# Performance work log

Hardware: AMD Instinct MI355X
Metric: run time of the kernel (lower is better)

## Reference

```python
import jax, jax.numpy as jnp
import numpy as np

B, S, E, H = 4, 2048, 1024, 16
D = E // H
MAX_DIST = 4
LN_EPS = 1e-5


def setup_inputs() -> dict:
    key = jax.random.key(0)
    ks = jax.random.split(key, 12)
    std = 1.0 / np.sqrt(E)
    inp = {
        "x": jax.random.normal(ks[0], (B, S, E), dtype=jnp.float32),
        "distances": jax.random.randint(ks[1], (B, S, S), 0, 5, dtype=jnp.int64),
        "Wq": jax.random.normal(ks[2], (E, E), dtype=jnp.float32) * std,
        "bq": jnp.zeros((E,), dtype=jnp.float32),
        "Wk": jax.random.normal(ks[3], (E, E), dtype=jnp.float32) * std,
        "bk": jnp.zeros((E,), dtype=jnp.float32),
        "Wv": jax.random.normal(ks[4], (E, E), dtype=jnp.float32) * std,
        "bv": jnp.zeros((E,), dtype=jnp.float32),
        "Wo": jax.random.normal(ks[5], (E, E), dtype=jnp.float32) * std,
        "bo": jnp.zeros((E,), dtype=jnp.float32),
        "dist_bias": jax.random.normal(ks[6], (MAX_DIST + 1,), dtype=jnp.float32) * 0.1,
        "ln_g": jnp.ones((E,), dtype=jnp.float32),
        "ln_b": jnp.zeros((E,), dtype=jnp.float32),
    }
    return inp


def _layernorm(y, g, b):
    mu = jnp.mean(y, axis=-1, keepdims=True)
    var = jnp.mean(jnp.square(y - mu), axis=-1, keepdims=True)
    return (y - mu) * jax.lax.rsqrt(var + LN_EPS) * g + b


def reference(x, distances, Wq, bq, Wk, bk, Wv, bv, Wo, bo, dist_bias, ln_g, ln_b):
    scale = 1.0 / np.sqrt(D)
    # projections (torch Linear: x @ W.T + b), split into heads -> [B,H,S,D]
    def heads(y):
        return y.reshape(B, S, H, D).transpose(0, 2, 1, 3)
    q = heads(x @ Wq.T + bq)
    k = heads(x @ Wk.T + bk)
    v = heads(x @ Wv.T + bv)
    scores = jnp.einsum('bhsd,bhtd->bhst', q, k) * scale  # [B,H,S,S]
    d = jnp.clip(distances, 0, MAX_DIST)
    bias = dist_bias[d]  # [B,S,S] gather from learned table
    scores = scores + bias[:, None, :, :]
    attn = jax.nn.softmax(scores, axis=-1)
    out = jnp.einsum('bhst,bhtd->bhsd', attn, v)
    out = out.transpose(0, 2, 1, 3).reshape(B, S, E)
    out = out @ Wo.T + bo
    return _layernorm(x + out, ln_g, ln_b)
```

## Files before the change

kernel.cpp:

```cpp
#include <hip/hip_runtime.h>
#include <stdint.h>

#define NB 4
#define NS 2048
#define NE 1024
#define NH 16
#define ND 64
#define LN_EPS 1e-5f
#define LN2I 1.44269504089f

typedef __attribute__((ext_vector_type(8))) unsigned short u16x8;
typedef __attribute__((ext_vector_type(4))) unsigned short u16x4;
typedef __attribute__((ext_vector_type(8))) short b16x8;
typedef __attribute__((ext_vector_type(4))) float f32x4;

static __device__ __forceinline__ unsigned short f2bf(float f) {
  unsigned u = __builtin_bit_cast(unsigned, f);
  u += 0x7FFFu + ((u >> 16) & 1u);
  return (unsigned short)(u >> 16);
}
static __device__ __forceinline__ float bf2f(unsigned short h) {
  return __builtin_bit_cast(float, (unsigned)h << 16);
}
static __device__ __forceinline__ float bperm_f(int addr, float v) {
  return __builtin_bit_cast(float,
      __builtin_amdgcn_ds_bpermute(addr, __builtin_bit_cast(int, v)));
}
static __device__ __forceinline__ unsigned cvtpk(float lo, float hi) {
  unsigned r;
  asm("v_cvt_pk_bf16_f32 %0, %1, %2" : "=v"(r) : "v"(lo), "v"(hi));
  return r;
}
#if __has_builtin(__builtin_amdgcn_exp2f)
static __device__ __forceinline__ float ex2(float x) { return __builtin_amdgcn_exp2f(x); }
#else
static __device__ __forceinline__ float ex2(float x) { return exp2f(x); }
#endif

static __device__ __forceinline__ void gload16(const unsigned short* gsrc,
                                               unsigned short* ldsbase) {
  __builtin_amdgcn_global_load_lds(
      (__attribute__((address_space(1))) unsigned int*)(uintptr_t)gsrc,
      (__attribute__((address_space(3))) unsigned int*)(uintptr_t)ldsbase,
      16, 0, 0);
}

#define MFMA16(a, b, c) __builtin_amdgcn_mfma_f32_16x16x32_bf16( \
    __builtin_bit_cast(b16x8, a), __builtin_bit_cast(b16x8, b), c, 0, 0, 0)

__global__ void k_cvt(const float* __restrict__ src, unsigned short* __restrict__ dst, int n) {
  int i = (blockIdx.x * 256 + threadIdx.x) * 8;
  if (i >= n) return;
  float4 a = *(const float4*)(src + i);
  float4 b = *(const float4*)(src + i + 4);
  u16x8 o;
  o[0]=f2bf(a.x); o[1]=f2bf(a.y); o[2]=f2bf(a.z); o[3]=f2bf(a.w);
  o[4]=f2bf(b.x); o[5]=f2bf(b.y); o[6]=f2bf(b.z); o[7]=f2bf(b.w);
  *(u16x8*)(dst + i) = o;
}

__global__ void k_bias(const int* __restrict__ d, const float* __restrict__ tbl,
                       unsigned short* __restrict__ bias) {
  size_t i = ((size_t)blockIdx.x * 256 + threadIdx.x) * 8;
  int4 a = *(const int4*)(d + i);
  int4 b = *(const int4*)(d + i + 4);
  u16x8 o;
  int v;
  v = a.x; v = v < 0 ? 0 : (v > 4 ? 4 : v); o[0] = f2bf(tbl[v] * LN2I);
  v = a.y; v = v < 0 ? 0 : (v > 4 ? 4 : v); o[1] = f2bf(tbl[v] * LN2I);
  v = a.z; v = v < 0 ? 0 : (v > 4 ? 4 : v); o[2] = f2bf(tbl[v] * LN2I);
  v = a.w; v = v < 0 ? 0 : (v > 4 ? 4 : v); o[3] = f2bf(tbl[v] * LN2I);
  v = b.x; v = v < 0 ? 0 : (v > 4 ? 4 : v); o[4] = f2bf(tbl[v] * LN2I);
  v = b.y; v = v < 0 ? 0 : (v > 4 ? 4 : v); o[5] = f2bf(tbl[v] * LN2I);
  v = b.z; v = v < 0 ? 0 : (v > 4 ? 4 : v); o[6] = f2bf(tbl[v] * LN2I);
  v = b.w; v = v < 0 ? 0 : (v > 4 ? 4 : v); o[7] = f2bf(tbl[v] * LN2I);
  *(u16x8*)(bias + i) = o;
}

__global__ __launch_bounds__(256, 3) void k_qkv(
    const unsigned short* __restrict__ xb,
    const unsigned short* __restrict__ wq, const unsigned short* __restrict__ wk_,
    const unsigned short* __restrict__ wv,
    const float* __restrict__ bq, const float* __restrict__ bk_, const float* __restrict__ bv,
    unsigned short* __restrict__ q, unsigned short* __restrict__ kk,
    unsigned short* __restrict__ vt) {
  __shared__ unsigned short sA[128 * 64];
  __shared__ unsigned short sB[128 * 64];
  const int tid = threadIdx.x;
  const int lane = tid & 63, wid = tid >> 6;
  const int g = lane >> 4, c16 = lane & 15;
  const int wm = wid >> 1, wn = wid & 1;
  const int z = blockIdx.z;
  const unsigned short* w = (z == 0) ? wq : ((z == 1) ? wk_ : wv);
  const float* bias = (z == 0) ? bq : ((z == 1) ? bk_ : bv);
  const int n0 = blockIdx.x * 128, m0 = blockIdx.y * 128;

  f32x4 acc[4][4];
#pragma unroll
  for (int i = 0; i < 4; ++i)
#pragma unroll
    for (int j = 0; j < 4; ++j) acc[i][j] = f32x4{0.f, 0.f, 0.f, 0.f};

  const int crow = lane >> 3, gcol8 = (lane & 7) * 8;

  for (int k0 = 0; k0 < NE; k0 += 64) {
#pragma unroll
    for (int i = 0; i < 4; ++i) {
      int c = wid * 4 + i;
      int row = c * 8 + crow;
      gload16(xb + (size_t)(m0 + row) * NE + k0 + gcol8, &sA[c * 512]);
      gload16(w + (size_t)(n0 + row) * NE + k0 + gcol8, &sB[c * 512]);
    }
    __syncthreads();
#pragma unroll
    for (int dc = 0; dc < 2; ++dc) {
      u16x8 af[4], bf[4];
#pragma unroll
      for (int mt = 0; mt < 4; ++mt)
        af[mt] = *(const u16x8*)(sA + (wm * 64 + mt * 16 + c16) * 64 + dc * 32 + g * 8);
#pragma unroll
      for (int nt = 0; nt < 4; ++nt)
        bf[nt] = *(const u16x8*)(sB + (wn * 64 + nt * 16 + c16) * 64 + dc * 32 + g * 8);
#pragma unroll
      for (int mt = 0; mt < 4; ++mt)
#pragma unroll
        for (int nt = 0; nt < 4; ++nt)
          acc[mt][nt] = MFMA16(af[mt], bf[nt], acc[mt][nt]);
    }
    __syncthreads();
  }

  if (z == 0) {
#pragma unroll
    for (int mt = 0; mt < 4; ++mt)
#pragma unroll
      for (int nt = 0; nt < 4; ++nt) {
        int col = n0 + wn * 64 + nt * 16 + c16;
        float bb = bias[col];
#pragma unroll
        for (int rr = 0; rr < 4; ++rr) {
          int row = m0 + wm * 64 + mt * 16 + g * 4 + rr;
          q[(size_t)row * NE + col] = f2bf(acc[mt][nt][rr] + bb);
        }
      }
  } else if (z == 1) {
#pragma unroll
    for (int mt = 0; mt < 4; ++mt)
#pragma unroll
      for (int nt = 0; nt < 4; ++nt) {
        int col = n0 + wn * 64 + nt * 16 + c16;
        float bb = bias[col];
        int seg = col & ~63, d = col & 63;
#pragma unroll
        for (int rr = 0; rr < 4; ++rr) {
          int row = m0 + wm * 64 + mt * 16 + g * 4 + rr;
          int dsw = (((d >> 3) ^ (row & 7)) << 3) | (d & 7);
          kk[(size_t)row * NE + seg + dsw] = f2bf(acc[mt][nt][rr] + bb);
        }
      }
  } else {
#pragma unroll
    for (int mt = 0; mt < 4; ++mt)
#pragma unroll
      for (int nt = 0; nt < 4; ++nt) {
        int col = n0 + wn * 64 + nt * 16 + c16;
        float bb = bias[col];
        int h = col >> 6, dd = col & 63;
        int grow = m0 + wm * 64 + mt * 16 + g * 4;
        int b = grow >> 11, ss = grow & 2047;
        int ssw = (ss & ~63) | (((((ss >> 3) & 7) ^ (dd & 7)) << 3)) | (ss & 7);
        u16x4 o;
#pragma unroll
        for (int rr = 0; rr < 4; ++rr) o[rr] = f2bf(acc[mt][nt][rr] + bb);
        *(u16x4*)(vt + ((size_t)((b * NH + h) * ND + dd)) * NS + ssw) = o;
      }
  }
}

__global__ __launch_bounds__(256, 2) void k_attn(
    const unsigned short* __restrict__ q, const unsigned short* __restrict__ kk,
    const unsigned short* __restrict__ vt, const unsigned short* __restrict__ bias,
    unsigned short* __restrict__ attn) {
  __shared__ unsigned short sK[2][64 * 64];
  __shared__ unsigned short sV[2][64 * 64];
  __shared__ unsigned short sP[4][16 * 64];
  const int tid = threadIdx.x, lane = tid & 63, wid = tid >> 6;
  const int g = lane >> 4, c16 = lane & 15;
  const int flat = blockIdx.x;
  const int kdec = flat >> 3;
  const int h = kdec & 15;
  const int G = (flat & 7) | ((kdec >> 4) << 3);
  const int b = G >> 3, qb = G & 7;
  const int q0 = qb * 256 + wid * 64;
  const size_t qkbase = ((size_t)b * NS) * NE + (size_t)h * ND;
  const size_t vbase = ((size_t)(b * NH + h) * ND) * NS;
  const size_t bbase = (size_t)b * NS * NS;
  unsigned short* sPw = &sP[wid][0];

  u16x8 qf[4][2];
#pragma unroll
  for (int mt = 0; mt < 4; ++mt)
#pragma unroll
    for (int dc = 0; dc < 2; ++dc)
      qf[mt][dc] = *(const u16x8*)(q + qkbase + (size_t)(q0 + mt * 16 + c16) * NE + dc * 32 + g * 8);

  f32x4 oa[4][4];
  float l[4];
#pragma unroll
  for (int mt = 0; mt < 4; ++mt) {
#pragma unroll
    for (int dt = 0; dt < 4; ++dt) oa[mt][dt] = f32x4{0.f, 0.f, 0.f, 0.f};
    l[mt] = 0.f;
  }

  int addr_rr[4];
#pragma unroll
  for (int rr = 0; rr < 4; ++rr) addr_rr[rr] = (g * 20 + rr) * 4;

  const int crow = lane >> 3, gcol8 = (lane & 7) * 8;
  const int rs0 = (g ^ (c16 & 7)) << 3;
  const int rs1 = ((4 + g) ^ (c16 & 7)) << 3;
  const int pw_base = c16 * 64 + (g & 1) * 4;
  const int pr0 = c16 * 64 + ((g ^ (c16 & 7)) << 3);
  const int pr1 = c16 * 64 + (((4 + g) ^ (c16 & 7)) << 3);

  u16x4 bp[4][4];

  auto stage = [&](int kt, int ib) {
#pragma unroll
    for (int i = 0; i < 4; ++i) {
      int c = wid * 4 + i;
      if (c < 8)
        gload16(kk + qkbase + (size_t)(kt + c * 8 + crow) * NE + gcol8, &sK[ib][c * 512]);
      else
        gload16(vt + vbase + (size_t)((c - 8) * 8 + crow) * NS + kt + gcol8, &sV[ib][(c - 8) * 512]);
    }
  };

  stage(0, 0);
#pragma unroll
  for (int mt = 0; mt < 4; ++mt)
#pragma unroll
    for (int nt = 0; nt < 4; ++nt)
      bp[mt][nt] = *(const u16x4*)(bias + bbase +
          (size_t)(q0 + mt * 16 + c16) * NS + 0 + nt * 16 + g * 4);

  for (int kt = 0, it = 0; kt < NS; kt += 64, ++it) {
    __syncthreads();
    if (kt + 64 < NS) stage(kt + 64, (it + 1) & 1);
    const unsigned short* bK = &sK[it & 1][0];
    const unsigned short* bV = &sV[it & 1][0];

    u16x8 kf[4][2];
#pragma unroll
    for (int nt = 0; nt < 4; ++nt) {
      const unsigned short* kr = bK + (nt * 16 + c16) * 64;
      kf[nt][0] = *(const u16x8*)(kr + rs0);
      kf[nt][1] = *(const u16x8*)(kr + rs1);
    }

#pragma unroll
    for (int mt = 0; mt < 4; ++mt) {
      f32x4 p[4];
      __builtin_amdgcn_s_setprio(1);
#pragma unroll
      for (int nt = 0; nt < 4; ++nt) {
        f32x4 t = f32x4{0.f, 0.f, 0.f, 0.f};
        t = MFMA16(kf[nt][0], qf[mt][0], t);
        t = MFMA16(kf[nt][1], qf[mt][1], t);
        p[nt] = t;
      }
      __builtin_amdgcn_s_setprio(0);
      float rs = 0.f;
#pragma unroll
      for (int nt = 0; nt < 4; ++nt)
#pragma unroll
        for (int rr = 0; rr < 4; ++rr) {
          float e = ex2(p[nt][rr] * (0.125f * LN2I) + bf2f(bp[mt][nt][rr]));
          p[nt][rr] = e;
          rs += e;
        }
      rs += __shfl_xor(rs, 16);
      rs += __shfl_xor(rs, 32);
      l[mt] += rs;
#pragma unroll
      for (int nt = 0; nt < 4; ++nt) {
        unsigned w0 = cvtpk(p[nt][0], p[nt][1]);
        unsigned w1 = cvtpk(p[nt][2], p[nt][3]);
        *(unsigned long long*)(sPw + pw_base + (((2 * nt + (g >> 1)) ^ (c16 & 7)) << 3)) =
            ((unsigned long long)w1 << 32) | (unsigned long long)w0;
      }
      if (mt == 1 && kt + 64 < NS) {
#pragma unroll
        for (int m2 = 0; m2 < 2; ++m2)
#pragma unroll
          for (int nt = 0; nt < 4; ++nt)
            bp[m2][nt] = *(const u16x4*)(bias + bbase +
                (size_t)(q0 + m2 * 16 + c16) * NS + kt + 64 + nt * 16 + g * 4);
      }
      if (mt == 3 && kt + 64 < NS) {
#pragma unroll
        for (int m2 = 0; m2 < 2; ++m2)
#pragma unroll
          for (int nt = 0; nt < 4; ++nt)
            bp[2 + m2][nt] = *(const u16x4*)(bias + bbase +
                (size_t)(q0 + (2 + m2) * 16 + c16) * NS + kt + 64 + nt * 16 + g * 4);
      }
      __builtin_amdgcn_s_setprio(1);
#pragma unroll
      for (int h2 = 0; h2 < 2; ++h2) {
        u16x8 pa = *(const u16x8*)(sPw + (h2 ? pr1 : pr0));
#pragma unroll
        for (int dt = 0; dt < 4; ++dt) {
          u16x8 vb = *(const u16x8*)(bV + (dt * 16 + c16) * 64 + (h2 ? rs1 : rs0));
          oa[mt][dt] = MFMA16(pa, vb, oa[mt][dt]);
        }
      }
      __builtin_amdgcn_s_setprio(0);
    }
  }

#pragma unroll
  for (int mt = 0; mt < 4; ++mt) {
    float invl = 1.0f / l[mt];
    float invr[4];
#pragma unroll
    for (int rr = 0; rr < 4; ++rr) invr[rr] = bperm_f(addr_rr[rr], invl);
#pragma unroll
    for (int dt = 0; dt < 4; ++dt)
#pragma unroll
      for (int rr = 0; rr < 4; ++rr) {
        int row = q0 + mt * 16 + g * 4 + rr;
        attn[qkbase + (size_t)row * NE + dt * 16 + c16] = f2bf(oa[mt][dt][rr] * invr[rr]);
      }
  }
}

__global__ __launch_bounds__(256, 3) void k_proj(
    const unsigned short* __restrict__ a, const unsigned short* __restrict__ w,
    const float* __restrict__ bo, const float* __restrict__ x, float* __restrict__ y) {
  __shared__ unsigned short sA[128 * 64];
  __shared__ unsigned short sB[128 * 64];
  const int tid = threadIdx.x;
  const int lane = tid & 63, wid = tid >> 6;
  const int g = lane >> 4, c16 = lane & 15;
  const int wm = wid >> 1, wn = wid & 1;
  const int n0 = blockIdx.x * 128, m0 = blockIdx.y * 128;

  f32x4 acc[4][4];
#pragma unroll
  for (int i = 0; i < 4; ++i)
#pragma unroll
    for (int j = 0; j < 4; ++j) acc[i][j] = f32x4{0.f, 0.f, 0.f, 0.f};

  const int crow = lane >> 3, gcol8 = (lane & 7) * 8;

  for (int k0 = 0; k0 < NE; k0 += 64) {
#pragma unroll
    for (int i = 0; i < 4; ++i) {
      int c = wid * 4 + i;
      int row = c * 8 + crow;
      gload16(a + (size_t)(m0 + row) * NE + k0 + gcol8, &sA[c * 512]);
      gload16(w + (size_t)(n0 + row) * NE + k0 + gcol8, &sB[c * 512]);
    }
    __syncthreads();
#pragma unroll
    for (int dc = 0; dc < 2; ++dc) {
      u16x8 af[4], bf[4];
#pragma unroll
      for (int mt = 0; mt < 4; ++mt)
        af[mt] = *(const u16x8*)(sA + (wm * 64 + mt * 16 + c16) * 64 + dc * 32 + g * 8);
#pragma unroll
      for (int nt = 0; nt < 4; ++nt)
        bf[nt] = *(const u16x8*)(sB + (wn * 64 + nt * 16 + c16) * 64 + dc * 32 + g * 8);
#pragma unroll
      for (int mt = 0; mt < 4; ++mt)
#pragma unroll
        for (int nt = 0; nt < 4; ++nt)
          acc[mt][nt] = MFMA16(af[mt], bf[nt], acc[mt][nt]);
    }
    __syncthreads();
  }

#pragma unroll
  for (int mt = 0; mt < 4; ++mt)
#pragma unroll
    for (int nt = 0; nt < 4; ++nt) {
      int col = n0 + wn * 64 + nt * 16 + c16;
      float bb = bo[col];
#pragma unroll
      for (int rr = 0; rr < 4; ++rr) {
        int row = m0 + wm * 64 + mt * 16 + g * 4 + rr;
        y[(size_t)row * NE + col] = acc[mt][nt][rr] + bb + x[(size_t)row * NE + col];
      }
    }
}

__global__ void k_ln(const float* __restrict__ y, const float* __restrict__ gg,
                     const float* __restrict__ bb, float* __restrict__ out) {
  const int row = blockIdx.x, tid = threadIdx.x;
  float4 v = *(const float4*)(y + (size_t)row * NE + tid * 4);
  float s = v.x + v.y + v.z + v.w;
  float s2 = v.x * v.x + v.y * v.y + v.z * v.z + v.w * v.w;
#pragma unroll
  for (int off = 1; off < 64; off <<= 1) {
    s += __shfl_xor(s, off);
    s2 += __shfl_xor(s2, off);
  }
  __shared__ float red[8];
  const int wid = tid >> 6, lane = tid & 63;
  if (lane == 0) { red[wid * 2] = s; red[wid * 2 + 1] = s2; }
  __syncthreads();
  s = red[0] + red[2] + red[4] + red[6];
  s2 = red[1] + red[3] + red[5] + red[7];
  float mu = s * (1.0f / NE);
  float var = s2 * (1.0f / NE) - mu * mu;
  float rstd = rsqrtf(var + LN_EPS);
  float4 g4 = *(const float4*)(gg + tid * 4);
  float4 b4 = *(const float4*)(bb + tid * 4);
  float4 o;
  o.x = (v.x - mu) * rstd * g4.x + b4.x;
  o.y = (v.y - mu) * rstd * g4.y + b4.y;
  o.z = (v.z - mu) * rstd * g4.z + b4.z;
  o.w = (v.w - mu) * rstd * g4.w + b4.w;
  *(float4*)(out + (size_t)row * NE + tid * 4) = o;
}

extern "C" void kernel_launch(void* const* d_in, const int* in_sizes, int n_in,
                              void* d_out, int out_size, void* d_ws, size_t ws_size,
                              hipStream_t stream) {
  (void)in_sizes; (void)n_in; (void)out_size; (void)ws_size;
  const float* x = (const float*)d_in[0];
  const int* dist = (const int*)d_in[1];
  const float* Wq = (const float*)d_in[2];
  const float* bq = (const float*)d_in[3];
  const float* Wk = (const float*)d_in[4];
  const float* bk = (const float*)d_in[5];
  const float* Wv = (const float*)d_in[6];
  const float* bv = (const float*)d_in[7];
  const float* Wo = (const float*)d_in[8];
  const float* bo = (const float*)d_in[9];
  const float* tbl = (const float*)d_in[10];
  const float* lng = (const float*)d_in[11];
  const float* lnb = (const float*)d_in[12];
  float* out = (float*)d_out;

  char* ws = (char*)d_ws;
  size_t off = 0;
  auto alloc = [&](size_t bytes) {
    char* p = ws + off;
    off += (bytes + 255) & ~(size_t)255;
    return p;
  };
  unsigned short* xb = (unsigned short*)d_out;
  unsigned short* wqb = (unsigned short*)alloc((size_t)NE * NE * 2);
  unsigned short* wkb = (unsigned short*)alloc((size_t)NE * NE * 2);
  unsigned short* wvb = (unsigned short*)alloc((size_t)NE * NE * 2);
  unsigned short* wob = (unsigned short*)alloc((size_t)NE * NE * 2);
  unsigned short* qq  = (unsigned short*)alloc((size_t)NB * NS * NE * 2);
  unsigned short* kb  = (unsigned short*)alloc((size_t)NB * NS * NE * 2);
  unsigned short* vtb = (unsigned short*)alloc((size_t)NB * NS * NE * 2);
  unsigned short* attn = (unsigned short*)alloc((size_t)NB * NS * NE * 2);
  unsigned short* bias = (unsigned short*)alloc((size_t)NB * NS * NS * 2);
  float* y = out;

  k_cvt<<<NB * NS * NE / 2048, 256, 0, stream>>>(x, xb, NB * NS * NE);
  k_cvt<<<NE * NE / 2048, 256, 0, stream>>>(Wq, wqb, NE * NE);
  k_cvt<<<NE * NE / 2048, 256, 0, stream>>>(Wk, wkb, NE * NE);
  k_cvt<<<NE * NE / 2048, 256, 0, stream>>>(Wv, wvb, NE * NE);
  k_cvt<<<NE * NE / 2048, 256, 0, stream>>>(Wo, wob, NE * NE);
  k_bias<<<(NB * NS * NS) / 2048, 256, 0, stream>>>(dist, tbl, bias);
  k_qkv<<<dim3(NE / 128, NB * NS / 128, 3), 256, 0, stream>>>(
      xb, wqb, wkb, wvb, bq, bk, bv, qq, kb, vtb);
  k_attn<<<dim3(NB * (NS / 256) * NH), 256, 0, stream>>>(qq, kb, vtb, bias, attn);
  k_proj<<<dim3(NE / 128, NB * NS / 128), 256, 0, stream>>>(attn, wob, bo, x, y);
  k_ln<<<NB * NS, 256, 0, stream>>>(y, lng, lnb, out);
}
```

Before: 302.0 us.

## Rewrite attention kernel with 32x32 MFMA and in-register P via permlane swap

The attention kernel moves from 16x16x32 to 32x32x16 bf16 MFMA, with each wave handling 32 query rows instead of 64. The softmax probabilities are repacked into the PV MFMA operand layout in registers with v_permlane32_swap, which removes the per-wave LDS scratch buffer for P and its write/read traffic. Blocks now cover 128 queries, so the grid doubles, and launch bounds raise occupancy to 4 blocks per CU. The trade-off is that K/V tiles are reloaded from global memory by twice as many blocks, and correctness depends on the permlane swap matching the MFMA operand layout.

Measured after the change: 511.8 us. +69.4%, slower.

```diff
diff --git a/kernel.cpp b/kernel.cpp
--- a/kernel.cpp
+++ b/kernel.cpp
@@ -13,6 +13,8 @@
 typedef __attribute__((ext_vector_type(4))) unsigned short u16x4;
 typedef __attribute__((ext_vector_type(8))) short b16x8;
 typedef __attribute__((ext_vector_type(4))) float f32x4;
+typedef __attribute__((ext_vector_type(16))) float f32x16;
+typedef __attribute__((ext_vector_type(4))) unsigned u32x4;
 
 static __device__ __forceinline__ unsigned short f2bf(float f) {
   unsigned u = __builtin_bit_cast(unsigned, f);
@@ -30,6 +32,9 @@
   unsigned r;
   asm("v_cvt_pk_bf16_f32 %0, %1, %2" : "=v"(r) : "v"(lo), "v"(hi));
   return r;
+}
+static __device__ __forceinline__ void plswap(unsigned &a, unsigned &b) {
+  asm("v_permlane32_swap_b32 %0, %1" : "+v"(a), "+v"(b));
 }
 #if __has_builtin(__builtin_amdgcn_exp2f)
 static __device__ __forceinline__ float ex2(float x) { return __builtin_amdgcn_exp2f(x); }
@@ -46,6 +51,8 @@
 }
 
 #define MFMA16(a, b, c) __builtin_amdgcn_mfma_f32_16x16x32_bf16( \
+    __builtin_bit_cast(b16x8, a), __builtin_bit_cast(b16x8, b), c, 0, 0, 0)
+#define MFMA32(a, b, c) __builtin_amdgcn_mfma_f32_32x32x16_bf16( \
     __builtin_bit_cast(b16x8, a), __builtin_bit_cast(b16x8, b), c, 0, 0, 0)
 
 __global__ void k_cvt(const float* __restrict__ src, unsigned short* __restrict__ dst, int n) {
@@ -177,54 +184,38 @@
   }
 }
 
-__global__ __launch_bounds__(256, 2) void k_attn(
+__global__ __launch_bounds__(256, 4) void k_attn(
     const unsigned short* __restrict__ q, const unsigned short* __restrict__ kk,
     const unsigned short* __restrict__ vt, const unsigned short* __restrict__ bias,
     unsigned short* __restrict__ attn) {
   __shared__ unsigned short sK[2][64 * 64];
   __shared__ unsigned short sV[2][64 * 64];
-  __shared__ unsigned short sP[4][16 * 64];
   const int tid = threadIdx.x, lane = tid & 63, wid = tid >> 6;
-  const int g = lane >> 4, c16 = lane & 15;
+  const int c32 = lane & 31, hi = lane >> 5;
   const int flat = blockIdx.x;
   const int kdec = flat >> 3;
   const int h = kdec & 15;
   const int G = (flat & 7) | ((kdec >> 4) << 3);
-  const int b = G >> 3, qb = G & 7;
-  const int q0 = qb * 256 + wid * 64;
+  const int b = G >> 4, qb = G & 15;
+  const int q0 = qb * 128 + wid * 32;
   const size_t qkbase = ((size_t)b * NS) * NE + (size_t)h * ND;
   const size_t vbase = ((size_t)(b * NH + h) * ND) * NS;
-  const size_t bbase = (size_t)b * NS * NS;
-  unsigned short* sPw = &sP[wid][0];
-
-  u16x8 qf[4][2];
-#pragma unroll
-  for (int mt = 0; mt < 4; ++mt)
-#pragma unroll
-    for (int dc = 0; dc < 2; ++dc)
-      qf[mt][dc] = *(const u16x8*)(q + qkbase + (size_t)(q0 + mt * 16 + c16) * NE + dc * 32 + g * 8);
-
-  f32x4 oa[4][4];
-  float l[4];
-#pragma unroll
-  for (int mt = 0; mt < 4; ++mt) {
-#pragma unroll
-    for (int dt = 0; dt < 4; ++dt) oa[mt][dt] = f32x4{0.f, 0.f, 0.f, 0.f};
-    l[mt] = 0.f;
-  }
-
-  int addr_rr[4];
-#pragma unroll
-  for (int rr = 0; rr < 4; ++rr) addr_rr[rr] = (g * 20 + rr) * 4;
+  const unsigned short* brow = bias + (size_t)b * NS * NS + (size_t)(q0 + c32) * NS;
+
+  u16x8 qf[4];
+#pragma unroll
+  for (int dc = 0; dc < 4; ++dc)
+    qf[dc] = *(const u16x8*)(q + qkbase + (size_t)(q0 + c32) * NE + dc * 16 + hi * 8);
+
+  f32x16 oa[2];
+#pragma unroll
+  for (int j = 0; j < 2; ++j)
+#pragma unroll
+    for (int i = 0; i < 16; ++i) oa[j][i] = 0.f;
+  float l = 0.f;
 
   const int crow = lane >> 3, gcol8 = (lane & 7) * 8;
-  const int rs0 = (g ^ (c16 & 7)) << 3;
-  const int rs1 = ((4 + g) ^ (c16 & 7)) << 3;
-  const int pw_base = c16 * 64 + (g & 1) * 4;
-  const int pr0 = c16 * 64 + ((g ^ (c16 & 7)) << 3);
-  const int pr1 = c16 * 64 + (((4 + g) ^ (c16 & 7)) << 3);
-
-  u16x4 bp[4][4];
+  const int swz = c32 & 7;
 
   auto stage = [&](int kt, int ib) {
 #pragma unroll
@@ -237,13 +228,11 @@
     }
   };
 
+  u16x4 bp[2][4];
   stage(0, 0);
 #pragma unroll
-  for (int mt = 0; mt < 4; ++mt)
-#pragma unroll
-    for (int nt = 0; nt < 4; ++nt)
-      bp[mt][nt] = *(const u16x4*)(bias + bbase +
-          (size_t)(q0 + mt * 16 + c16) * NS + 0 + nt * 16 + g * 4);
+  for (int k8 = 0; k8 < 4; ++k8)
+    bp[0][k8] = *(const u16x4*)(brow + k8 * 8 + 4 * hi);
 
   for (int kt = 0, it = 0; kt < NS; kt += 64, ++it) {
     __syncthreads();
@@ -251,88 +240,70 @@
     const unsigned short* bK = &sK[it & 1][0];
     const unsigned short* bV = &sV[it & 1][0];
 
-    u16x8 kf[4][2];
-#pragma unroll
-    for (int nt = 0; nt < 4; ++nt) {
-      const unsigned short* kr = bK + (nt * 16 + c16) * 64;
-      kf[nt][0] = *(const u16x8*)(kr + rs0);
-      kf[nt][1] = *(const u16x8*)(kr + rs1);
-    }
-
-#pragma unroll
-    for (int mt = 0; mt < 4; ++mt) {
-      f32x4 p[4];
+    u32x4 pa[4];
+#pragma unroll
+    for (int ts = 0; ts < 2; ++ts) {
+      if (ts == 0) {
+#pragma unroll
+        for (int k8 = 0; k8 < 4; ++k8)
+          bp[1][k8] = *(const u16x4*)(brow + kt + 32 + k8 * 8 + 4 * hi);
+      } else if (kt + 64 < NS) {
+#pragma unroll
+        for (int k8 = 0; k8 < 4; ++k8)
+          bp[0][k8] = *(const u16x4*)(brow + kt + 64 + k8 * 8 + 4 * hi);
+      }
+      u16x8 kf[4];
+#pragma unroll
+      for (int dc = 0; dc < 4; ++dc)
+        kf[dc] = *(const u16x8*)(bK + (ts * 32 + c32) * 64 + (((dc * 2 + hi) ^ swz) << 3));
+      f32x16 s;
+#pragma unroll
+      for (int i = 0; i < 16; ++i) s[i] = 0.f;
       __builtin_amdgcn_s_setprio(1);
 #pragma unroll
-      for (int nt = 0; nt < 4; ++nt) {
-        f32x4 t = f32x4{0.f, 0.f, 0.f, 0.f};
-        t = MFMA16(kf[nt][0], qf[mt][0], t);
-        t = MFMA16(kf[nt][1], qf[mt][1], t);
-        p[nt] = t;
-      }
+      for (int dc = 0; dc < 4; ++dc) s = MFMA32(kf[dc], qf[dc], s);
       __builtin_amdgcn_s_setprio(0);
       float rs = 0.f;
 #pragma unroll
-      for (int nt = 0; nt < 4; ++nt)
-#pragma unroll
-        for (int rr = 0; rr < 4; ++rr) {
-          float e = ex2(p[nt][rr] * (0.125f * LN2I) + bf2f(bp[mt][nt][rr]));
-          p[nt][rr] = e;
-          rs += e;
-        }
-      rs += __shfl_xor(rs, 16);
-      rs += __shfl_xor(rs, 32);
-      l[mt] += rs;
-#pragma unroll
-      for (int nt = 0; nt < 4; ++nt) {
-        unsigned w0 = cvtpk(p[nt][0], p[nt][1]);
-        unsigned w1 = cvtpk(p[nt][2], p[nt][3]);
-        *(unsigned long long*)(sPw + pw_base + (((2 * nt + (g >> 1)) ^ (c16 & 7)) << 3)) =
-            ((unsigned long long)w1 << 32) | (unsigned long long)w0;
-      }
-      if (mt == 1 && kt + 64 < NS) {
-#pragma unroll
-        for (int m2 = 0; m2 < 2; ++m2)
-#pragma unroll
-          for (int nt = 0; nt < 4; ++nt)
-            bp[m2][nt] = *(const u16x4*)(bias + bbase +
-                (size_t)(q0 + m2 * 16 + c16) * NS + kt + 64 + nt * 16 + g * 4);
-      }
-      if (mt == 3 && kt + 64 < NS) {
-#pragma unroll
-        for (int m2 = 0; m2 < 2; ++m2)
-#pragma unroll
-          for (int nt = 0; nt < 4; ++nt)
-            bp[2 + m2][nt] = *(const u16x4*)(bias + bbase +
-                (size_t)(q0 + (2 + m2) * 16 + c16) * NS + kt + 64 + nt * 16 + g * 4);
-      }
-      __builtin_amdgcn_s_setprio(1);
-#pragma unroll
-      for (int h2 = 0; h2 < 2; ++h2) {
-        u16x8 pa = *(const u16x8*)(sPw + (h2 ? pr1 : pr0));
-#pragma unroll
-        for (int dt = 0; dt < 4; ++dt) {
-          u16x8 vb = *(const u16x8*)(bV + (dt * 16 + c16) * 64 + (h2 ? rs1 : rs0));
-          oa[mt][dt] = MFMA16(pa, vb, oa[mt][dt]);
-        }
-      }
-      __builtin_amdgcn_s_setprio(0);
-    }
-  }
-
-#pragma unroll
-  for (int mt = 0; mt < 4; ++mt) {
-    float invl = 1.0f / l[mt];
-    float invr[4];
-#pragma unroll
-    for (int rr = 0; rr < 4; ++rr) invr[rr] = bperm_f(addr_rr[rr], invl);
-#pragma unroll
-    for (int dt = 0; dt < 4; ++dt)
-#pragma unroll
-      for (int rr = 0; rr < 4; ++rr) {
-        int row = q0 + mt * 16 + g * 4 + rr;
-        attn[qkbase + (size_t)row * NE + dt * 16 + c16] = f2bf(oa[mt][dt][rr] * invr[rr]);
-      }
+      for (int r = 0; r < 16; ++r) {
+        float e = ex2(s[r] * (0.125f * LN2I) + bf2f(bp[ts][r >> 2][r & 3]));
+        s[r] = e;
+        rs += e;
+      }
+      l += rs;
+      {
+        unsigned u0 = cvtpk(s[0], s[1]), u1 = cvtpk(s[2], s[3]);
+        unsigned u2 = cvtpk(s[4], s[5]), u3 = cvtpk(s[6], s[7]);
+        plswap(u0, u2);
+        plswap(u1, u3);
+        pa[ts * 2] = (u32x4){u0, u1, u2, u3};
+        unsigned u4 = cvtpk(s[8], s[9]), u5 = cvtpk(s[10], s[11]);
+        unsigned u6 = cvtpk(s[12], s[13]), u7 = cvtpk(s[14], s[15]);
+        plswap(u4, u6);
+        plswap(u5, u7);
+        pa[ts * 2 + 1] = (u32x4){u4, u5, u6, u7};
+      }
+    }
+    __builtin_amdgcn_s_setprio(1);
+#pragma unroll
+    for (int dcol = 0; dcol < 2; ++dcol)
+#pragma unroll
+      for (int kc = 0; kc < 4; ++kc) {
+        u16x8 vf = *(const u16x8*)(bV + (dcol * 32 + c32) * 64 + (((kc * 2 + hi) ^ swz) << 3));
+        oa[dcol] = MFMA32(pa[kc], vf, oa[dcol]);
+      }
+    __builtin_amdgcn_s_setprio(0);
+  }
+
+  float lt = l + __shfl_xor(l, 32);
+  float invl = 1.0f / lt;
+#pragma unroll
+  for (int r = 0; r < 16; ++r) {
+    int qrow = (r & 3) + 8 * (r >> 2) + 4 * hi;
+    float inv_r = bperm_f(qrow << 2, invl);
+#pragma unroll
+    for (int dcol = 0; dcol < 2; ++dcol)
+      attn[qkbase + (size_t)(q0 + qrow) * NE + dcol * 32 + c32] = f2bf(oa[dcol][r] * inv_r);
   }
 }
 
@@ -472,7 +443,7 @@
   k_bias<<<(NB * NS * NS) / 2048, 256, 0, stream>>>(dist, tbl, bias);
   k_qkv<<<dim3(NE / 128, NB * NS / 128, 3), 256, 0, stream>>>(
       xb, wqb, wkb, wvb, bq, bk, bv, qq, kb, vtb);
-  k_attn<<<dim3(NB * (NS / 256) * NH), 256, 0, stream>>>(qq, kb, vtb, bias, attn);
+  k_attn<<<dim3(NB * (NS / 128) * NH), 256, 0, stream>>>(qq, kb, vtb, bias, attn);
   k_proj<<<dim3(NE / 128, NB * NS / 128), 256, 0, stream>>>(attn, wob, bo, x, y);
   k_ln<<<NB * NS, 256, 0, stream>>>(y, lng, lnb, out);
 }
```
